# Optimization experiments

Hardware: AMD Instinct MI355X
Metric: run time of the kernel (lower is better)

## Reference

```python
import jax, jax.numpy as jnp
import numpy as np

H = 16      # q heads
G = 4       # groups (n_rep)
THETA = 10000.0


def _rope(x, cos, sin):
    # x pairs adjacent elements (torch complex view of reshape(..., -1, 2))
    x0 = x[..., ::2]
    x1 = x[..., 1::2]
    r0 = x0 * cos - x1 * sin
    r1 = x0 * sin + x1 * cos
    return jnp.stack([r0, r1], axis=-1).reshape(x.shape)


def setup_inputs() -> dict:
    key = jax.random.key(0)
    ks = jax.random.split(key, 5)
    B, S, D = 2, 2048, 1024
    return {
        "x": jax.random.normal(ks[0], (B, S, D), jnp.float32),
        "Wq": jax.random.normal(ks[1], (D, D), jnp.float32) * 0.02,
        "Wk": jax.random.normal(ks[2], (D, D // G), jnp.float32) * 0.02,
        "Wv": jax.random.normal(ks[3], (D, D // G), jnp.float32) * 0.02,
        "Wo": jax.random.normal(ks[4], (D, D), jnp.float32) * 0.02,
    }


def reference(x, Wq, Wk, Wv, Wo):
    B, S, D = x.shape
    hd = D // H                     # head dim = 64
    Hkv = H // G                    # kv heads = 4

    q = x @ Wq                      # (B,S,D)
    k = x @ Wk                      # (B,S,D/G)
    v = x @ Wv                      # (B,S,D/G)

    # repeat_kv: (B,S,Hkv,hd) -> (B,S,H,hd)
    k = jnp.repeat(k.reshape(B, S, Hkv, hd), G, axis=2)
    v = jnp.repeat(v.reshape(B, S, Hkv, hd), G, axis=2)

    # RoPE angles: freqs precomputed over hidden_dim (as in source)
    inv = 1.0 / (THETA ** (jnp.arange(0, D, 2, dtype=jnp.float32) / D))  # (D/2,)
    ang = jnp.arange(S, dtype=jnp.float32)[:, None] * inv[None, :]       # (S,D/2)
    q = _rope(q, jnp.cos(ang)[None], jnp.sin(ang)[None])                 # (B,S,D)
    angk = ang[:, : hd // 2]                                             # (S,hd/2)
    k = _rope(k, jnp.cos(angk)[None, :, None, :], jnp.sin(angk)[None, :, None, :])

    q = q.reshape(B, S, H, hd).transpose(0, 2, 1, 3)   # (B,H,S,hd)
    k = k.transpose(0, 2, 1, 3)
    v = v.transpose(0, 2, 1, 3)

    # NOTE: scale uses sqrt(hidden_dim), faithful to source
    scores = jnp.einsum('bhqd,bhkd->bhqk', q, k) / jnp.sqrt(jnp.float32(D))
    p = jax.nn.softmax(scores, axis=-1)
    o = jnp.einsum('bhqk,bhkd->bhqd', p, v)
    o = o.transpose(0, 2, 1, 3).reshape(B, S, D)
    return o @ Wo
```

## Files before the change

### kernel.cpp

```cpp
#include <hip/hip_runtime.h>
#include <math.h>

#define BATCH 2
#define SEQ   2048
#define DMODEL 1024
#define KDIM  1024
#define NH    16
#define HDIM  64
#define GRP   4
#define NKV   4
#define NSPLIT 2

enum { M_PLAIN = 0, M_QKV = 1 };

#define LN_THETA 9.210340371976184f

typedef short bf8_t __attribute__((ext_vector_type(8)));
typedef float f4_t __attribute__((ext_vector_type(4)));
typedef unsigned short us4_t __attribute__((ext_vector_type(4)));
typedef unsigned short us8_t __attribute__((ext_vector_type(8)));

#define QB_OFF 0
#define KB_OFF 4194304
#define VB_OFF (4194304 + 1048576)

__device__ __forceinline__ unsigned short f2bf(float f) {
  unsigned int u = __float_as_uint(f);
  u += 0x7fffu + ((u >> 16) & 1u);
  return (unsigned short)(u >> 16);
}

__device__ __forceinline__ void gload_lds16(const void* g, void* l) {
  typedef __attribute__((address_space(1))) unsigned int gu32;
  typedef __attribute__((address_space(3))) unsigned int lu32;
  __builtin_amdgcn_global_load_lds((const gu32*)g, (lu32*)l, 16, 0, 0);
}

__global__ __launch_bounds__(256) void conv_x(const float* __restrict__ in,
                                              unsigned short* __restrict__ out) {
  const int i = blockIdx.x * 256 + threadIdx.x;
  float4 v = ((const float4*)in)[i];
  us4_t o = {f2bf(v.x), f2bf(v.y), f2bf(v.z), f2bf(v.w)};
  ((us4_t*)out)[i] = o;
}

__global__ __launch_bounds__(256) void convT_all(const float* __restrict__ W0,
                                                 const float* __restrict__ W1,
                                                 const float* __restrict__ W2,
                                                 const float* __restrict__ W3,
                                                 unsigned short* __restrict__ Wqkvt,
                                                 unsigned short* __restrict__ Wot) {
  const float* W; unsigned short* out; int N, rowoff;
  switch (blockIdx.z) {
    case 0: W = W0; out = Wqkvt; N = 1024; rowoff = 0;    break;
    case 1: W = W1; out = Wqkvt; N = 256;  rowoff = 1024; break;
    case 2: W = W2; out = Wqkvt; N = 256;  rowoff = 1280; break;
    default: W = W3; out = Wot;  N = 1024; rowoff = 0;    break;
  }
  const int n0 = blockIdx.x * 64;
  if (n0 >= N) return;
  __shared__ unsigned short T[64][72];
  const int t = threadIdx.x;
  const int k0 = blockIdx.y * 64;
  const int kr = t >> 4, n4 = (t & 15) * 4;
#pragma unroll
  for (int i = 0; i < 4; ++i) {
    const int k = kr + i * 16;
    float4 v = *(const float4*)&W[(size_t)(k0 + k) * N + n0 + n4];
    T[n4 + 0][k] = f2bf(v.x);
    T[n4 + 1][k] = f2bf(v.y);
    T[n4 + 2][k] = f2bf(v.z);
    T[n4 + 3][k] = f2bf(v.w);
  }
  __syncthreads();
#pragma unroll
  for (int i = 0; i < 2; ++i) {
    const int c = t + i * 256;
    const int n = c >> 3, kc = (c & 7) * 8;
    us8_t v = *(const us8_t*)&T[n][kc];
    *(us8_t*)&out[(size_t)(rowoff + n0 + n) * KDIM + k0 + kc] = v;
  }
}

template <int MODE>
__global__ __launch_bounds__(256, 3) void gemm_bf16(const unsigned short* __restrict__ A,
                                                    const unsigned short* __restrict__ Bt,
                                                    void* __restrict__ Cdst_, int N) {
  __shared__ __align__(16) unsigned short As[64 * 64];
  __shared__ __align__(16) unsigned short Bs[128 * 64];

  const int tid = threadIdx.x;
  const int lane = tid & 63, quad = lane >> 4, l16 = lane & 15;
  const int w = tid >> 6, wm = w >> 1, wn = w & 1;
  const int row0 = blockIdx.x * 64, col0 = blockIdx.y * 128;

  const int m0 = tid >> 2;
  const int kc0 = (tid & 3) ^ ((m0 >> 1) & 3);
  const unsigned short* Ag0 = A + (size_t)(row0 + m0) * KDIM + kc0 * 8;
  const unsigned short* Bg0 = Bt + (size_t)(col0 + m0) * KDIM + kc0 * 8;
  unsigned short* Al0 = &As[tid * 8];
  unsigned short* Bl0 = &Bs[tid * 8];

  int aoff[2][2], boff[4][2];
#pragma unroll
  for (int mi = 0; mi < 2; ++mi) {
    const int am = wm * 32 + mi * 16 + l16;
    const int sw = quad ^ ((am >> 1) & 3);
#pragma unroll
    for (int kh = 0; kh < 2; ++kh)
      aoff[mi][kh] = kh * 2048 + (((am << 2) | sw) << 3);
  }
#pragma unroll
  for (int ni = 0; ni < 4; ++ni) {
    const int bn = wn * 64 + ni * 16 + l16;
    const int sw = quad ^ ((bn >> 1) & 3);
#pragma unroll
    for (int kh = 0; kh < 2; ++kh)
      boff[ni][kh] = kh * 4096 + (((bn << 2) | sw) << 3);
  }

  f4_t acc[2][4];
#pragma unroll
  for (int mi = 0; mi < 2; ++mi)
#pragma unroll
    for (int ni = 0; ni < 4; ++ni) acc[mi][ni] = (f4_t){0.f, 0.f, 0.f, 0.f};

  for (int kb = 0; kb < KDIM; kb += 64) {
    __syncthreads();
    gload_lds16(Ag0 + kb,       Al0);
    gload_lds16(Ag0 + kb + 32,  Al0 + 2048);
    gload_lds16(Bg0 + kb,                     Bl0);
    gload_lds16(Bg0 + (size_t)64 * KDIM + kb, Bl0 + 2048);
    gload_lds16(Bg0 + kb + 32,                     Bl0 + 4096);
    gload_lds16(Bg0 + (size_t)64 * KDIM + kb + 32, Bl0 + 6144);
    __syncthreads();

    bf8_t af[2][2], bfr[4][2];
#pragma unroll
    for (int mi = 0; mi < 2; ++mi)
#pragma unroll
      for (int kh = 0; kh < 2; ++kh) af[mi][kh] = *(const bf8_t*)&As[aoff[mi][kh]];
#pragma unroll
    for (int ni = 0; ni < 4; ++ni)
#pragma unroll
      for (int kh = 0; kh < 2; ++kh) bfr[ni][kh] = *(const bf8_t*)&Bs[boff[ni][kh]];
#pragma unroll
    for (int kh = 0; kh < 2; ++kh)
#pragma unroll
      for (int mi = 0; mi < 2; ++mi)
#pragma unroll
        for (int ni = 0; ni < 4; ++ni)
          acc[mi][ni] = __builtin_amdgcn_mfma_f32_16x16x32_bf16(af[mi][kh], bfr[ni][kh], acc[mi][ni], 0, 0, 0);
  }

  if constexpr (MODE == M_PLAIN) {
    float* out = (float*)Cdst_;
#pragma unroll
    for (int mi = 0; mi < 2; ++mi) {
      const int rowb = row0 + wm * 32 + mi * 16 + quad * 4;
#pragma unroll
      for (int ni = 0; ni < 4; ++ni) {
        const int n = col0 + wn * 64 + ni * 16 + l16;
#pragma unroll
        for (int r = 0; r < 4; ++r)
          out[(size_t)(rowb + r) * N + n] = acc[mi][ni][r];
      }
    }
  } else {
    unsigned short* Qb = (unsigned short*)Cdst_;
    unsigned short* Kb = Qb + (KB_OFF - QB_OFF);
    unsigned short* Vb = Qb + (VB_OFF - QB_OFF);
#pragma unroll
    for (int ni = 0; ni < 4; ++ni) {
      const int nb = col0 + wn * 64 + ni * 16;
      const int n = nb + l16;
      if (nb < 1024) {
        const float inv = expf(-(float)(2 * (n >> 1)) * (LN_THETA / (float)DMODEL));
        const float sgn = (n & 1) ? 1.f : -1.f;
        const int h = n >> 6, d = n & 63;
#pragma unroll
        for (int mi = 0; mi < 2; ++mi) {
          const int rowb = row0 + wm * 32 + mi * 16 + quad * 4;
#pragma unroll
          for (int r = 0; r < 4; ++r) {
            const int row = rowb + r;
            const int bb = row >> 11, s = row & (SEQ - 1);
            const float v = acc[mi][ni][r];
            const float p = __shfl_xor(v, 1);
            float sn, cs;
            sincosf((float)s * inv, &sn, &cs);
            const float res = (v * cs + sgn * p * sn) * 0.03125f;
            Qb[((size_t)(bb * NH + h) * SEQ + s) * HDIM + d] = f2bf(res);
          }
        }
      } else if (nb < 1280) {
        const int nk = n - 1024;
        const int hkv = nk >> 6, d = nk & 63;
        const float inv = expf(-(float)(2 * (d >> 1)) * (LN_THETA / (float)DMODEL));
        const float sgn = (nk & 1) ? 1.f : -1.f;
#pragma unroll
        for (int mi = 0; mi < 2; ++mi) {
          const int rowb = row0 + wm * 32 + mi * 16 + quad * 4;
#pragma unroll
          for (int r = 0; r < 4; ++r) {
            const int row = rowb + r;
            const int bb = row >> 11, s = row & (SEQ - 1);
            const float v = acc[mi][ni][r];
            const float p = __shfl_xor(v, 1);
            float sn, cs;
            sincosf((float)s * inv, &sn, &cs);
            const float res = v * cs + sgn * p * sn;
            Kb[((size_t)(bb * NKV + hkv) * SEQ + s) * HDIM + d] = f2bf(res);
          }
        }
      } else {
        const int nv = n - 1280;
        const int hkv = nv >> 6, d = nv & 63;
#pragma unroll
        for (int mi = 0; mi < 2; ++mi) {
          const int s0 = row0 + wm * 32 + mi * 16 + quad * 4;
          const int bb = s0 >> 11, s = s0 & (SEQ - 1);
          us4_t st = {f2bf(acc[mi][ni][0]), f2bf(acc[mi][ni][1]),
                      f2bf(acc[mi][ni][2]), f2bf(acc[mi][ni][3])};
          *(us4_t*)&Vb[((size_t)(bb * NKV + hkv) * HDIM + d) * SEQ + s] = st;
        }
      }
    }
  }
}

__global__ __launch_bounds__(256, 4) void attn_fwd(const unsigned short* __restrict__ Q,
                                                   const unsigned short* __restrict__ K,
                                                   const unsigned short* __restrict__ V,
                                                   float* __restrict__ Opart,
                                                   float* __restrict__ Lpart) {
  __shared__ __align__(16) unsigned short Kt[4096];
  __shared__ __align__(16) unsigned short Vt[4096];
  __shared__ __align__(16) unsigned short Pt[4][2048];

  const int b = blockIdx.x >> 4;
  const int h = blockIdx.x & (NH - 1);
  const int hkv = h >> 2;
  const int q0 = blockIdx.y * 128;
  const int sp = blockIdx.z;
  const int tid = threadIdx.x;
  const int w = tid >> 6;
  const int lane = tid & 63;
  const int quad = lane >> 4;
  const int l16 = lane & 15;

  const unsigned short* Qg = Q + ((size_t)(b * NH + h) * SEQ + q0 + w * 32) * HDIM;
  const unsigned short* Kg = K + (size_t)(b * NKV + hkv) * SEQ * HDIM;
  const unsigned short* Vg = V + (size_t)(b * NKV + hkv) * HDIM * SEQ;

  bf8_t qb[2][2];
#pragma unroll
  for (int g = 0; g < 2; ++g)
#pragma unroll
    for (int half = 0; half < 2; ++half)
      qb[g][half] = *(const bf8_t*)(Qg + (size_t)(g * 16 + l16) * HDIM + half * 32 + quad * 8);

  f4_t accO[2][4];
#pragma unroll
  for (int g = 0; g < 2; ++g)
#pragma unroll
    for (int d = 0; d < 4; ++d) accO[g][d] = (f4_t){0.f, 0.f, 0.f, 0.f};
  float accLs[2] = {0.f, 0.f};

  const int x7 = l16 & 7;
  const int kc0 = (quad ^ x7) << 3;
  const int kc1 = kc0 ^ 32;
  unsigned short* Ptw = Pt[w];

  const int srow0 = tid >> 3, sch = tid & 7;
  const int gcol = ((sch ^ (srow0 & 7)) << 3);
  const unsigned short* KgA = Kg + (size_t)srow0 * HDIM + gcol;
  const unsigned short* VgA = Vg + (size_t)srow0 * SEQ + gcol;

  const int kbeg = sp * (SEQ / NSPLIT);
  const int kend = kbeg + SEQ / NSPLIT;
  for (int k0 = kbeg; k0 < kend; k0 += 64) {
    __syncthreads();
    gload_lds16(KgA + (size_t)k0 * HDIM, &Kt[tid * 8]);
    gload_lds16(KgA + (size_t)(k0 + 32) * HDIM, &Kt[tid * 8 + 2048]);
    gload_lds16(VgA + k0, &Vt[tid * 8]);
    gload_lds16(VgA + k0 + 32 * SEQ, &Vt[tid * 8 + 2048]);
    __syncthreads();

#pragma unroll
    for (int cb = 0; cb < 4; ++cb) {
      const int krow = (cb * 16 + l16) * 64;
      bf8_t kf0 = *(const bf8_t*)&Kt[krow + kc0];
      bf8_t kf1 = *(const bf8_t*)&Kt[krow + kc1];
      const int pcol = (((cb * 2 + (quad >> 1)) ^ x7) << 3) + ((quad & 1) << 2);
#pragma unroll
      for (int g = 0; g < 2; ++g) {
        f4_t s = (f4_t){0.f, 0.f, 0.f, 0.f};
        s = __builtin_amdgcn_mfma_f32_16x16x32_bf16(kf0, qb[g][0], s, 0, 0, 0);
        s = __builtin_amdgcn_mfma_f32_16x16x32_bf16(kf1, qb[g][1], s, 0, 0, 0);
        const float p0 = __expf(s[0]), p1 = __expf(s[1]);
        const float p2 = __expf(s[2]), p3 = __expf(s[3]);
        accLs[g] += (p0 + p1) + (p2 + p3);
        uint2 pk;
        pk.x = __builtin_amdgcn_perm(__float_as_uint(p1) + 0x8000u,
                                     __float_as_uint(p0) + 0x8000u, 0x07060302u);
        pk.y = __builtin_amdgcn_perm(__float_as_uint(p3) + 0x8000u,
                                     __float_as_uint(p2) + 0x8000u, 0x07060302u);
        *(uint2*)&Ptw[(g * 16 + l16) * 64 + pcol] = pk;
      }
    }

    bf8_t pa[2][2];
#pragma unroll
    for (int g = 0; g < 2; ++g) {
      const int prow = (g * 16 + l16) * 64;
      pa[g][0] = *(const bf8_t*)&Ptw[prow + kc0];
      pa[g][1] = *(const bf8_t*)&Ptw[prow + kc1];
    }
#pragma unroll
    for (int db = 0; db < 4; ++db) {
      const int vrow = (db * 16 + l16) * 64;
      bf8_t vf0 = *(const bf8_t*)&Vt[vrow + kc0];
      bf8_t vf1 = *(const bf8_t*)&Vt[vrow + kc1];
#pragma unroll
      for (int g = 0; g < 2; ++g) {
        accO[g][db] = __builtin_amdgcn_mfma_f32_16x16x32_bf16(pa[g][0], vf0, accO[g][db], 0, 0, 0);
        accO[g][db] = __builtin_amdgcn_mfma_f32_16x16x32_bf16(pa[g][1], vf1, accO[g][db], 0, 0, 0);
      }
    }
  }

#pragma unroll
  for (int g = 0; g < 2; ++g) {
    accLs[g] += __shfl_xor(accLs[g], 16);
    accLs[g] += __shfl_xor(accLs[g], 32);
  }
  float* Lsh = (float*)Ptw;
  if (quad == 0) {
    Lsh[l16] = accLs[0];
    Lsh[16 + l16] = accLs[1];
  }
  float4 lrow[2];
  lrow[0] = *(const float4*)&Lsh[quad * 4];
  lrow[1] = *(const float4*)&Lsh[16 + quad * 4];

  float* Osp = Opart + (size_t)sp * BATCH * SEQ * NH * HDIM;
  float* Lsp = Lpart + (size_t)sp * BATCH * SEQ * NH;
#pragma unroll
  for (int g = 0; g < 2; ++g)
#pragma unroll
    for (int r = 0; r < 4; ++r) {
      const int q = q0 + w * 32 + g * 16 + quad * 4 + r;
      const size_t rowi = ((size_t)b * SEQ + q) * NH + h;
      float* op = Osp + rowi * HDIM;
#pragma unroll
      for (int db = 0; db < 4; ++db)
        op[db * 16 + l16] = accO[g][db][r];
      (void)lrow;
    }
  if (quad == 0) {
#pragma unroll
    for (int g = 0; g < 2; ++g) {
      const int q = q0 + w * 32 + g * 16 + l16;
      Lsp[((size_t)b * SEQ + q) * NH + h] = accLs[g];
    }
  }
}

__global__ __launch_bounds__(256) void attn_merge(const float* __restrict__ Opart,
                                                  const float* __restrict__ Lpart,
                                                  unsigned short* __restrict__ Ow) {
  const int idx = blockIdx.x * 256 + threadIdx.x;
  const int g = idx >> 4, j = (idx & 15) * 4;
  const size_t nq = (size_t)BATCH * SEQ * NH;
  float4 o0 = *(const float4*)&Opart[(size_t)g * HDIM + j];
  float4 o1 = *(const float4*)&Opart[nq * HDIM + (size_t)g * HDIM + j];
  const float il = 1.0f / (Lpart[g] + Lpart[nq + g]);
  us4_t o = {f2bf((o0.x + o1.x) * il), f2bf((o0.y + o1.y) * il),
             f2bf((o0.z + o1.z) * il), f2bf((o0.w + o1.w) * il)};
  *(us4_t*)&Ow[(size_t)g * HDIM + j] = o;
}

extern "C" void kernel_launch(void* const* d_in, const int* in_sizes, int n_in,
                              void* d_out, int out_size, void* d_ws, size_t ws_size,
                              hipStream_t stream) {
  (void)in_sizes; (void)n_in; (void)out_size; (void)ws_size;
  const float* x  = (const float*)d_in[0];
  const float* Wq = (const float*)d_in[1];
  const float* Wk = (const float*)d_in[2];
  const float* Wv = (const float*)d_in[3];
  const float* Wo = (const float*)d_in[4];
  float* out = (float*)d_out;

  unsigned short* Qb    = (unsigned short*)d_ws;
  unsigned short* Kb    = Qb + 4194304;
  unsigned short* Vb    = Kb + 1048576;
  unsigned short* xb    = Vb + 1048576;
  unsigned short* Owb   = xb + 4194304;
  unsigned short* Wqkvt = Owb + 4194304;
  unsigned short* Wot   = Wqkvt + 1572864;
  float* Opart = (float*)(Wot + 1048576);
  float* Lpart = Opart + (size_t)NSPLIT * 4194304;

  dim3 blk(256);
  conv_x<<<dim3(4096), blk, 0, stream>>>(x, xb);
  convT_all<<<dim3(16, 16, 4), blk, 0, stream>>>(Wq, Wk, Wv, Wo, Wqkvt, Wot);

  gemm_bf16<M_QKV><<<dim3(64, 12), blk, 0, stream>>>(xb, Wqkvt, Qb, 1536);
  attn_fwd<<<dim3(BATCH * NH, SEQ / 128, NSPLIT), blk, 0, stream>>>(Qb, Kb, Vb, Opart, Lpart);
  attn_merge<<<dim3(4096), blk, 0, stream>>>(Opart, Lpart, Owb);
  gemm_bf16<M_PLAIN><<<dim3(64, 8), blk, 0, stream>>>(Owb, Wot, out, DMODEL);
}
```

Before: 178.1 us.

## Keep softmax probabilities in registers and permute V reads to match MFMA layout

```diff
diff --git a/kernel.cpp b/kernel.cpp
--- a/kernel.cpp
+++ b/kernel.cpp
@@ -236,7 +236,6 @@
                                                    float* __restrict__ Lpart) {
   __shared__ __align__(16) unsigned short Kt[4096];
   __shared__ __align__(16) unsigned short Vt[4096];
-  __shared__ __align__(16) unsigned short Pt[4][2048];
 
   const int b = blockIdx.x >> 4;
   const int h = blockIdx.x & (NH - 1);
@@ -270,7 +269,15 @@
   const int x7 = l16 & 7;
   const int kc0 = (quad ^ x7) << 3;
   const int kc1 = kc0 ^ 32;
-  unsigned short* Ptw = Pt[w];
+
+  int vi[2][2];
+#pragma unroll
+  for (int kh = 0; kh < 2; ++kh) {
+    const int c0 = kh * 4 + (quad >> 1);
+    vi[kh][0] = (((c0) ^ x7) << 1) | (quad & 1);
+    vi[kh][1] = (((c0 + 2) ^ x7) << 1) | (quad & 1);
+  }
+  const unsigned long long* Vt64 = (const unsigned long long*)Vt;
 
   const int srow0 = tid >> 3, sch = tid & 7;
   const int gcol = ((sch ^ (srow0 & 7)) << 3);
@@ -287,45 +294,51 @@
     gload_lds16(VgA + k0 + 32 * SEQ, &Vt[tid * 8 + 2048]);
     __syncthreads();
 
+    float p[2][4][4];
 #pragma unroll
     for (int cb = 0; cb < 4; ++cb) {
       const int krow = (cb * 16 + l16) * 64;
       bf8_t kf0 = *(const bf8_t*)&Kt[krow + kc0];
       bf8_t kf1 = *(const bf8_t*)&Kt[krow + kc1];
-      const int pcol = (((cb * 2 + (quad >> 1)) ^ x7) << 3) + ((quad & 1) << 2);
 #pragma unroll
       for (int g = 0; g < 2; ++g) {
         f4_t s = (f4_t){0.f, 0.f, 0.f, 0.f};
         s = __builtin_amdgcn_mfma_f32_16x16x32_bf16(kf0, qb[g][0], s, 0, 0, 0);
         s = __builtin_amdgcn_mfma_f32_16x16x32_bf16(kf1, qb[g][1], s, 0, 0, 0);
-        const float p0 = __expf(s[0]), p1 = __expf(s[1]);
-        const float p2 = __expf(s[2]), p3 = __expf(s[3]);
-        accLs[g] += (p0 + p1) + (p2 + p3);
-        uint2 pk;
-        pk.x = __builtin_amdgcn_perm(__float_as_uint(p1) + 0x8000u,
-                                     __float_as_uint(p0) + 0x8000u, 0x07060302u);
-        pk.y = __builtin_amdgcn_perm(__float_as_uint(p3) + 0x8000u,
-                                     __float_as_uint(p2) + 0x8000u, 0x07060302u);
-        *(uint2*)&Ptw[(g * 16 + l16) * 64 + pcol] = pk;
+#pragma unroll
+        for (int r = 0; r < 4; ++r) p[g][cb][r] = __expf(s[r]);
+        accLs[g] += (p[g][cb][0] + p[g][cb][1]) + (p[g][cb][2] + p[g][cb][3]);
       }
     }
 
-    bf8_t pa[2][2];
-#pragma unroll
-    for (int g = 0; g < 2; ++g) {
-      const int prow = (g * 16 + l16) * 64;
-      pa[g][0] = *(const bf8_t*)&Ptw[prow + kc0];
-      pa[g][1] = *(const bf8_t*)&Ptw[prow + kc1];
-    }
+    union { bf8_t bf; unsigned int dw[4]; } pa[2][2];
+#pragma unroll
+    for (int g = 0; g < 2; ++g)
+#pragma unroll
+      for (int kh = 0; kh < 2; ++kh) {
+#pragma unroll
+        for (int half = 0; half < 2; ++half) {
+          const int cb = kh * 2 + half;
+          pa[g][kh].dw[half * 2 + 0] =
+              __builtin_amdgcn_perm(__float_as_uint(p[g][cb][1]) + 0x8000u,
+                                    __float_as_uint(p[g][cb][0]) + 0x8000u, 0x07060302u);
+          pa[g][kh].dw[half * 2 + 1] =
+              __builtin_amdgcn_perm(__float_as_uint(p[g][cb][3]) + 0x8000u,
+                                    __float_as_uint(p[g][cb][2]) + 0x8000u, 0x07060302u);
+        }
+      }
+
 #pragma unroll
     for (int db = 0; db < 4; ++db) {
-      const int vrow = (db * 16 + l16) * 64;
-      bf8_t vf0 = *(const bf8_t*)&Vt[vrow + kc0];
-      bf8_t vf1 = *(const bf8_t*)&Vt[vrow + kc1];
-#pragma unroll
-      for (int g = 0; g < 2; ++g) {
-        accO[g][db] = __builtin_amdgcn_mfma_f32_16x16x32_bf16(pa[g][0], vf0, accO[g][db], 0, 0, 0);
-        accO[g][db] = __builtin_amdgcn_mfma_f32_16x16x32_bf16(pa[g][1], vf1, accO[g][db], 0, 0, 0);
+      const int row16 = (db * 16 + l16) * 16;
+#pragma unroll
+      for (int kh = 0; kh < 2; ++kh) {
+        union { bf8_t bf; unsigned long long u[2]; } vf;
+        vf.u[0] = Vt64[row16 + vi[kh][0]];
+        vf.u[1] = Vt64[row16 + vi[kh][1]];
+#pragma unroll
+        for (int g = 0; g < 2; ++g)
+          accO[g][db] = __builtin_amdgcn_mfma_f32_16x16x32_bf16(pa[g][kh].bf, vf.bf, accO[g][db], 0, 0, 0);
       }
     }
   }
@@ -335,14 +348,6 @@
     accLs[g] += __shfl_xor(accLs[g], 16);
     accLs[g] += __shfl_xor(accLs[g], 32);
   }
-  float* Lsh = (float*)Ptw;
-  if (quad == 0) {
-    Lsh[l16] = accLs[0];
-    Lsh[16 + l16] = accLs[1];
-  }
-  float4 lrow[2];
-  lrow[0] = *(const float4*)&Lsh[quad * 4];
-  lrow[1] = *(const float4*)&Lsh[16 + quad * 4];
 
   float* Osp = Opart + (size_t)sp * BATCH * SEQ * NH * HDIM;
   float* Lsp = Lpart + (size_t)sp * BATCH * SEQ * NH;
@@ -356,7 +361,6 @@
 #pragma unroll
       for (int db = 0; db < 4; ++db)
         op[db * 16 + l16] = accO[g][db][r];
-      (void)lrow;
     }
   if (quad == 0) {
 #pragma unroll
```

After: 173.3 us. 2.7% less time.

## Keep P in registers via permuted V layout, fp16 partials, split keys four ways

Applied to the files above, without the earlier changes.

```diff
diff --git a/kernel.cpp b/kernel.cpp
--- a/kernel.cpp
+++ b/kernel.cpp
@@ -9,7 +9,7 @@
 #define HDIM  64
 #define GRP   4
 #define NKV   4
-#define NSPLIT 2
+#define NSPLIT 4
 
 enum { M_PLAIN = 0, M_QKV = 1 };
 
@@ -19,6 +19,8 @@
 typedef float f4_t __attribute__((ext_vector_type(4)));
 typedef unsigned short us4_t __attribute__((ext_vector_type(4)));
 typedef unsigned short us8_t __attribute__((ext_vector_type(8)));
+typedef _Float16 h_t;
+typedef _Float16 h4_t __attribute__((ext_vector_type(4)));
 
 #define QB_OFF 0
 #define KB_OFF 4194304
@@ -219,24 +221,25 @@
 #pragma unroll
         for (int mi = 0; mi < 2; ++mi) {
           const int s0 = row0 + wm * 32 + mi * 16 + quad * 4;
-          const int bb = s0 >> 11, s = s0 & (SEQ - 1);
-          us4_t st = {f2bf(acc[mi][ni][0]), f2bf(acc[mi][ni][1]),
-                      f2bf(acc[mi][ni][2]), f2bf(acc[mi][ni][3])};
-          *(us4_t*)&Vb[((size_t)(bb * NKV + hkv) * HDIM + d) * SEQ + s] = st;
+          const int bb = s0 >> 11, sl = s0 & (SEQ - 1);
+          const int st = sl & 63;
+          const int ps = (sl & ~63) | (st & 0x20) | ((st & 0x0C) << 1) | ((st & 0x10) >> 2);
+          us4_t stv = {f2bf(acc[mi][ni][0]), f2bf(acc[mi][ni][1]),
+                       f2bf(acc[mi][ni][2]), f2bf(acc[mi][ni][3])};
+          *(us4_t*)&Vb[((size_t)(bb * NKV + hkv) * HDIM + d) * SEQ + ps] = stv;
         }
       }
     }
   }
 }
 
-__global__ __launch_bounds__(256, 4) void attn_fwd(const unsigned short* __restrict__ Q,
+__global__ __launch_bounds__(256, 6) void attn_fwd(const unsigned short* __restrict__ Q,
                                                    const unsigned short* __restrict__ K,
                                                    const unsigned short* __restrict__ V,
-                                                   float* __restrict__ Opart,
+                                                   h_t* __restrict__ Opart,
                                                    float* __restrict__ Lpart) {
   __shared__ __align__(16) unsigned short Kt[4096];
   __shared__ __align__(16) unsigned short Vt[4096];
-  __shared__ __align__(16) unsigned short Pt[4][2048];
 
   const int b = blockIdx.x >> 4;
   const int h = blockIdx.x & (NH - 1);
@@ -267,32 +270,29 @@
     for (int d = 0; d < 4; ++d) accO[g][d] = (f4_t){0.f, 0.f, 0.f, 0.f};
   float accLs[2] = {0.f, 0.f};
 
-  const int x7 = l16 & 7;
-  const int kc0 = (quad ^ x7) << 3;
-  const int kc1 = kc0 ^ 32;
-  unsigned short* Ptw = Pt[w];
-
-  const int srow0 = tid >> 3, sch = tid & 7;
-  const int gcol = ((sch ^ (srow0 & 7)) << 3);
-  const unsigned short* KgA = Kg + (size_t)srow0 * HDIM + gcol;
-  const unsigned short* VgA = Vg + (size_t)srow0 * SEQ + gcol;
+  const int sw8 = (quad ^ ((l16 >> 1) & 3)) << 3;
+
+  const int skey = tid >> 2;
+  const int gc = ((tid & 3) ^ ((tid >> 3) & 3)) << 3;
+  const unsigned short* KgA = Kg + (size_t)skey * HDIM + gc;
+  const unsigned short* VgA = Vg + (size_t)skey * SEQ + gc;
 
   const int kbeg = sp * (SEQ / NSPLIT);
   const int kend = kbeg + SEQ / NSPLIT;
   for (int k0 = kbeg; k0 < kend; k0 += 64) {
     __syncthreads();
-    gload_lds16(KgA + (size_t)k0 * HDIM, &Kt[tid * 8]);
-    gload_lds16(KgA + (size_t)(k0 + 32) * HDIM, &Kt[tid * 8 + 2048]);
-    gload_lds16(VgA + k0, &Vt[tid * 8]);
-    gload_lds16(VgA + k0 + 32 * SEQ, &Vt[tid * 8 + 2048]);
+    gload_lds16(KgA + (size_t)k0 * HDIM,      &Kt[tid * 8]);
+    gload_lds16(KgA + (size_t)k0 * HDIM + 32, &Kt[tid * 8 + 2048]);
+    gload_lds16(VgA + k0,      &Vt[tid * 8]);
+    gload_lds16(VgA + k0 + 32, &Vt[tid * 8 + 2048]);
     __syncthreads();
 
+    union { bf8_t bf; unsigned int dw[4]; } pa[2][2];
 #pragma unroll
     for (int cb = 0; cb < 4; ++cb) {
-      const int krow = (cb * 16 + l16) * 64;
-      bf8_t kf0 = *(const bf8_t*)&Kt[krow + kc0];
-      bf8_t kf1 = *(const bf8_t*)&Kt[krow + kc1];
-      const int pcol = (((cb * 2 + (quad >> 1)) ^ x7) << 3) + ((quad & 1) << 2);
+      const int koff = (cb * 16 + l16) * 32 + sw8;
+      bf8_t kf0 = *(const bf8_t*)&Kt[koff];
+      bf8_t kf1 = *(const bf8_t*)&Kt[koff + 2048];
 #pragma unroll
       for (int g = 0; g < 2; ++g) {
         f4_t s = (f4_t){0.f, 0.f, 0.f, 0.f};
@@ -301,31 +301,24 @@
         const float p0 = __expf(s[0]), p1 = __expf(s[1]);
         const float p2 = __expf(s[2]), p3 = __expf(s[3]);
         accLs[g] += (p0 + p1) + (p2 + p3);
-        uint2 pk;
-        pk.x = __builtin_amdgcn_perm(__float_as_uint(p1) + 0x8000u,
-                                     __float_as_uint(p0) + 0x8000u, 0x07060302u);
-        pk.y = __builtin_amdgcn_perm(__float_as_uint(p3) + 0x8000u,
-                                     __float_as_uint(p2) + 0x8000u, 0x07060302u);
-        *(uint2*)&Ptw[(g * 16 + l16) * 64 + pcol] = pk;
+        pa[g][cb >> 1].dw[(cb & 1) * 2 + 0] =
+            __builtin_amdgcn_perm(__float_as_uint(p1) + 0x8000u,
+                                  __float_as_uint(p0) + 0x8000u, 0x07060302u);
+        pa[g][cb >> 1].dw[(cb & 1) * 2 + 1] =
+            __builtin_amdgcn_perm(__float_as_uint(p3) + 0x8000u,
+                                  __float_as_uint(p2) + 0x8000u, 0x07060302u);
       }
     }
 
-    bf8_t pa[2][2];
-#pragma unroll
-    for (int g = 0; g < 2; ++g) {
-      const int prow = (g * 16 + l16) * 64;
-      pa[g][0] = *(const bf8_t*)&Ptw[prow + kc0];
-      pa[g][1] = *(const bf8_t*)&Ptw[prow + kc1];
-    }
 #pragma unroll
     for (int db = 0; db < 4; ++db) {
-      const int vrow = (db * 16 + l16) * 64;
-      bf8_t vf0 = *(const bf8_t*)&Vt[vrow + kc0];
-      bf8_t vf1 = *(const bf8_t*)&Vt[vrow + kc1];
+      const int voff = (db * 16 + l16) * 32 + sw8;
+      bf8_t vf0 = *(const bf8_t*)&Vt[voff];
+      bf8_t vf1 = *(const bf8_t*)&Vt[voff + 2048];
 #pragma unroll
       for (int g = 0; g < 2; ++g) {
-        accO[g][db] = __builtin_amdgcn_mfma_f32_16x16x32_bf16(pa[g][0], vf0, accO[g][db], 0, 0, 0);
-        accO[g][db] = __builtin_amdgcn_mfma_f32_16x16x32_bf16(pa[g][1], vf1, accO[g][db], 0, 0, 0);
+        accO[g][db] = __builtin_amdgcn_mfma_f32_16x16x32_bf16(pa[g][0].bf, vf0, accO[g][db], 0, 0, 0);
+        accO[g][db] = __builtin_amdgcn_mfma_f32_16x16x32_bf16(pa[g][1].bf, vf1, accO[g][db], 0, 0, 0);
       }
     }
   }
@@ -335,16 +328,8 @@
     accLs[g] += __shfl_xor(accLs[g], 16);
     accLs[g] += __shfl_xor(accLs[g], 32);
   }
-  float* Lsh = (float*)Ptw;
-  if (quad == 0) {
-    Lsh[l16] = accLs[0];
-    Lsh[16 + l16] = accLs[1];
-  }
-  float4 lrow[2];
-  lrow[0] = *(const float4*)&Lsh[quad * 4];
-  lrow[1] = *(const float4*)&Lsh[16 + quad * 4];
-
-  float* Osp = Opart + (size_t)sp * BATCH * SEQ * NH * HDIM;
+
+  h_t* Osp = Opart + (size_t)sp * BATCH * SEQ * NH * HDIM;
   float* Lsp = Lpart + (size_t)sp * BATCH * SEQ * NH;
 #pragma unroll
   for (int g = 0; g < 2; ++g)
@@ -352,11 +337,10 @@
     for (int r = 0; r < 4; ++r) {
       const int q = q0 + w * 32 + g * 16 + quad * 4 + r;
       const size_t rowi = ((size_t)b * SEQ + q) * NH + h;
-      float* op = Osp + rowi * HDIM;
+      h_t* op = Osp + rowi * HDIM;
 #pragma unroll
       for (int db = 0; db < 4; ++db)
-        op[db * 16 + l16] = accO[g][db][r];
-      (void)lrow;
+        op[db * 16 + l16] = (h_t)accO[g][db][r];
     }
   if (quad == 0) {
 #pragma unroll
@@ -367,17 +351,23 @@
   }
 }
 
-__global__ __launch_bounds__(256) void attn_merge(const float* __restrict__ Opart,
+__global__ __launch_bounds__(256) void attn_merge(const h_t* __restrict__ Opart,
                                                   const float* __restrict__ Lpart,
                                                   unsigned short* __restrict__ Ow) {
   const int idx = blockIdx.x * 256 + threadIdx.x;
   const int g = idx >> 4, j = (idx & 15) * 4;
   const size_t nq = (size_t)BATCH * SEQ * NH;
-  float4 o0 = *(const float4*)&Opart[(size_t)g * HDIM + j];
-  float4 o1 = *(const float4*)&Opart[nq * HDIM + (size_t)g * HDIM + j];
-  const float il = 1.0f / (Lpart[g] + Lpart[nq + g]);
-  us4_t o = {f2bf((o0.x + o1.x) * il), f2bf((o0.y + o1.y) * il),
-             f2bf((o0.z + o1.z) * il), f2bf((o0.w + o1.w) * il)};
+  float L = 0.f;
+  float4 acc = make_float4(0.f, 0.f, 0.f, 0.f);
+#pragma unroll
+  for (int u = 0; u < NSPLIT; ++u) {
+    L += Lpart[u * nq + g];
+    h4_t o = *(const h4_t*)&Opart[((size_t)u * nq + g) * HDIM + j];
+    acc.x += (float)o[0]; acc.y += (float)o[1];
+    acc.z += (float)o[2]; acc.w += (float)o[3];
+  }
+  const float il = 1.0f / L;
+  us4_t o = {f2bf(acc.x * il), f2bf(acc.y * il), f2bf(acc.z * il), f2bf(acc.w * il)};
   *(us4_t*)&Ow[(size_t)g * HDIM + j] = o;
 }
 
@@ -399,8 +389,8 @@
   unsigned short* Owb   = xb + 4194304;
   unsigned short* Wqkvt = Owb + 4194304;
   unsigned short* Wot   = Wqkvt + 1572864;
-  float* Opart = (float*)(Wot + 1048576);
-  float* Lpart = Opart + (size_t)NSPLIT * 4194304;
+  h_t* Opart = (h_t*)(Wot + 1048576);
+  float* Lpart = (float*)(Opart + (size_t)NSPLIT * 4194304);
 
   dim3 blk(256);
   conv_x<<<dim3(4096), blk, 0, stream>>>(x, xb);
```

After: 319.9 us. 79.7% more time.
